# Kernel tuning notes

Measured on AMD Instinct MI355X. Metric: run time of the kernel, lower is better.

Reference implementation:

```python
import jax, jax.numpy as jnp
import numpy as np

T_NUM = 1024      # tracks
DET_NUM = 1024    # detections
DEG = 64          # candidate detections per track
E = T_NUM * DEG   # directed track->det edges (row<col half)
N = T_NUM + DET_NUM
D_IN = 512
D_EMB = 256
LAM = 5.0
SLACK = -0.2
SINKHORN_ITERS = 8


def setup_inputs() -> dict:
    key = jax.random.key(0)
    ks = jax.random.split(key, 20)
    x = jax.random.normal(ks[0], (N, D_IN), jnp.float32)
    coords = jax.random.uniform(ks[1], (N, 4), dtype=jnp.float32)
    r = jax.random.uniform(ks[2], (N, 4), dtype=jnp.float32)
    bx1 = r[:, 0] * 100.0; by1 = r[:, 1] * 100.0
    bw = r[:, 2] * 50.0 + 1.0; bh = r[:, 3] * 50.0 + 1.0
    coords_original = jnp.stack([bx1, by1, bx1 + bw, by1 + bh], axis=1)
    src_t = jnp.repeat(jnp.arange(T_NUM, dtype=jnp.int32), DEG)
    off = jnp.tile(jnp.arange(DEG, dtype=jnp.int32), T_NUM)
    dst_d = (src_t * 13 + off) % DET_NUM            # unique det per (track, slot)
    src = src_t
    dst = dst_d + T_NUM                              # detection node ids come after tracks
    edge_index = jnp.concatenate([jnp.stack([src, dst]), jnp.stack([dst, src])], axis=1)
    ground_truth = jax.random.bernoulli(ks[3], 0.1, (T_NUM * DET_NUM,)).astype(jnp.float32)

    def lin(k, i, o):
        return jax.random.normal(k, (i, o), jnp.float32) / np.sqrt(i).astype(np.float32)

    params = {
        'W_enc': lin(ks[4], D_IN, D_EMB), 'b_enc': jnp.zeros((D_EMB,), jnp.float32),
        'W1a': lin(ks[5], 2 * D_EMB, 64), 'b1a': jnp.zeros((64,), jnp.float32),
        'W2a': lin(ks[6], 64, 1), 'b2a': jnp.zeros((1,), jnp.float32),
        'W1g': lin(ks[7], 8, 16), 'b1g': jnp.zeros((16,), jnp.float32),
        'W2g': lin(ks[8], 16, 1), 'b2g': jnp.zeros((1,), jnp.float32),
        'W1f': lin(ks[9], 2, 8), 'b1f': jnp.zeros((8,), jnp.float32),
        'W2f': lin(ks[10], 8, 1), 'b2f': jnp.zeros((1,), jnp.float32),
        'Wn': lin(ks[11], D_EMB, D_EMB), 'Wm': lin(ks[12], D_EMB, D_EMB),
        'bo': jnp.zeros((D_EMB,), jnp.float32),
        'W1c': lin(ks[13], 2, 8), 'b1c': jnp.zeros((8,), jnp.float32),
        'W2c': lin(ks[14], 8, 1), 'b2c': jnp.zeros((1,), jnp.float32),
    }
    out = {'x': x, 'coords': coords, 'coords_original': coords_original,
           'ground_truth': ground_truth, 'edge_index': edge_index}
    out.update(params)
    return out


def _box_iou(a, b):
    # a, b: [E, 4] boxes (x1, y1, x2, y2)
    lt = jnp.maximum(a[:, :2], b[:, :2])
    rb = jnp.minimum(a[:, 2:], b[:, 2:])
    wh = jnp.clip(rb - lt, 0.0)
    inter = wh[:, 0] * wh[:, 1]
    area_a = (a[:, 2] - a[:, 0]) * (a[:, 3] - a[:, 1])
    area_b = (b[:, 2] - b[:, 0]) * (b[:, 3] - b[:, 1])
    return inter / (area_a + area_b - inter + 1e-9)


def _sinkhorn(M):
    def body(M, _):
        M = M / (jnp.sum(M, axis=1, keepdims=True) + 1e-9)
        M = M / (jnp.sum(M, axis=0, keepdims=True) + 1e-9)
        return M, None
    M, _ = jax.lax.scan(body, M, None, length=SINKHORN_ITERS)
    return M


def _forward(x, coords, coords_original,
             W_enc, b_enc, W1a, b1a, W2a, b2a, W1g, b1g, W2g, b2g,
             W1f, b1f, W2f, b2f, Wn, Wm, bo, W1c, b1c, W2c, b2c,
             edge_index):
    node = jax.nn.relu(x @ W_enc + b_enc)                      # [N, D_EMB]
    src, dst = edge_index[0], edge_index[1]                    # [2E]
    # batched per-edge appearance affinity (replaces python edge loop)
    pair = jnp.concatenate([node[src], node[dst]], axis=1)     # [2E, 2*D_EMB]
    a1 = jax.nn.relu(pair @ W1a + b1a) @ W2a + b2a             # [2E, 1]
    geo = jnp.concatenate([coords[src], coords[dst]], axis=1)  # [2E, 8]
    a2 = jax.nn.relu(geo @ W1g + b1g) @ W2g + b2g              # [2E, 1]
    e_in = jnp.concatenate([a1, a2], axis=1)                   # [2E, 2]
    edge_emb = jax.nn.relu(e_in @ W1f + b1f) @ W2f + b2f       # [2E, 1]
    # optim_net: one round of edge-weighted message passing
    msg = jax.ops.segment_sum(edge_emb * node[src], dst, num_segments=N)
    out = jax.nn.relu(node @ Wn + msg @ Wm + bo)               # [N, D_EMB]
    # forward (row < col) edges are the first E entries by construction
    sf, df = src[:E], dst[:E]
    oa, ob = out[sf], out[df]
    denom = jnp.maximum(jnp.linalg.norm(oa, axis=1) * jnp.linalg.norm(ob, axis=1), 1e-6)
    cosv = jnp.sum(oa * ob, axis=1) / denom                    # CosineSimilarity(dim=0) per edge
    iou = _box_iou(coords_original[sf], coords_original[df])   # [E]
    f_in = jnp.stack([cosv, iou], axis=1)                      # [E, 2]
    aff = (jax.nn.relu(f_in @ W1c + b1c) @ W2c + b2c)[:, 0]    # [E]
    # assignment matrix with slack row/col, scatter exp(aff*lam)
    slack_val = jnp.exp(jnp.float32(SLACK * LAM))
    M = jnp.full((T_NUM + 1, DET_NUM + 1), slack_val, jnp.float32)
    M = M.at[:T_NUM, :DET_NUM].set(0.0)
    M = M.at[sf, df - T_NUM].set(jnp.exp(aff * LAM))
    M = _sinkhorn(M)
    return M[:-1, :-1].reshape(-1)                             # [T_NUM*DET_NUM]


def reference(x, coords, coords_original, ground_truth, edge_index,
              W_enc, b_enc, W1a, b1a, W2a, b2a, W1g, b1g, W2g, b2g,
              W1f, b1f, W2f, b2f, Wn, Wm, bo, W1c, b1c, W2c, b2c):
    normalized_output = _forward(x, coords, coords_original,
                                 W_enc, b_enc, W1a, b1a, W2a, b2a,
                                 W1g, b1g, W2g, b2g, W1f, b1f, W2f, b2f,
                                 Wn, Wm, bo, W1c, b1c, W2c, b2c, edge_index)
    det_num = jnp.asarray(DET_NUM, jnp.int32)
    tracklet_num = jnp.asarray(T_NUM, jnp.int32)
    return (normalized_output, ground_truth, det_num, tracklet_num)
```

## Files before the change

kernel.cpp:

```cpp
#include <hip/hip_runtime.h>

#define T_NUM 1024
#define DET_NUM 1024
#define E_NUM 65536
#define TWO_E 131072
#define N_NODES 2048
#define D_IN 512
#define D_EMB 256

__device__ __forceinline__ unsigned bf16r(float x) {
  const unsigned u = __float_as_uint(x);
  return (u + 0x7fffu + ((u >> 16) & 1u)) >> 16;
}
__device__ __forceinline__ float bflo(unsigned p) { return __uint_as_float(p << 16); }
__device__ __forceinline__ float bfhi(unsigned p) { return __uint_as_float(p & 0xffff0000u); }

__global__ __launch_bounds__(1024) void k_enc_pg(
    const float* __restrict__ x, const float* __restrict__ W,
    const float* __restrict__ b, const float* __restrict__ coords,
    const float* __restrict__ W1a, const float* __restrict__ W1g,
    float* __restrict__ node, float* __restrict__ P1, float* __restrict__ P2,
    float* __restrict__ G1, float* __restrict__ G2) {
  __shared__ __align__(16) float ns[8][D_EMB];
  __shared__ __align__(16) float psq[3][8][D_EMB];
  __shared__ float pp1[8][64], pp2[8][64];
  const int tid = threadIdx.x;
  const int j = tid & 255;
  const int q = __builtin_amdgcn_readfirstlane(tid >> 8);
  const int row0 = blockIdx.x * 8;
  float acc[8];
  const float bj = b[j];
#pragma unroll
  for (int r = 0; r < 8; r++) acc[r] = (q == 0) ? bj : 0.f;
  const float* xr = x + (size_t)row0 * D_IN + q * 128;
  const float* Wp = W + (size_t)q * 128 * D_EMB;
  for (int k = 0; k < 128; k += 4) {
    const float w0 = Wp[(k + 0) * D_EMB + j];
    const float w1 = Wp[(k + 1) * D_EMB + j];
    const float w2 = Wp[(k + 2) * D_EMB + j];
    const float w3 = Wp[(k + 3) * D_EMB + j];
#pragma unroll
    for (int r = 0; r < 8; r++) {
      const float4 xv = *reinterpret_cast<const float4*>(xr + (size_t)r * D_IN + k);
      acc[r] = fmaf(xv.x, w0, acc[r]);
      acc[r] = fmaf(xv.y, w1, acc[r]);
      acc[r] = fmaf(xv.z, w2, acc[r]);
      acc[r] = fmaf(xv.w, w3, acc[r]);
    }
  }
  if (q > 0) {
#pragma unroll
    for (int r = 0; r < 8; r++) psq[q - 1][r][j] = acc[r];
  }
  __syncthreads();
  if (q == 0) {
#pragma unroll
    for (int r = 0; r < 8; r++) {
      const float v = fmaxf(acc[r] + psq[0][r][j] + psq[1][r][j] + psq[2][r][j], 0.f);
      node[(size_t)(row0 + r) * D_EMB + j] = v;
      ns[r][j] = v;
    }
  }
  __syncthreads();
  const int r2 = tid >> 7, q2 = (tid >> 6) & 1, hh = tid & 63;
  float a1 = 0.f, a2 = 0.f;
  {
    const int k0 = q2 * 128;
    for (int k = 0; k < 128; k += 4) {
      const float4 nv = *reinterpret_cast<const float4*>(&ns[r2][k0 + k]);
      a1 = fmaf(nv.x, W1a[(k0 + k + 0) * 64 + hh], a1);
      a1 = fmaf(nv.y, W1a[(k0 + k + 1) * 64 + hh], a1);
      a1 = fmaf(nv.z, W1a[(k0 + k + 2) * 64 + hh], a1);
      a1 = fmaf(nv.w, W1a[(k0 + k + 3) * 64 + hh], a1);
      a2 = fmaf(nv.x, W1a[(D_EMB + k0 + k + 0) * 64 + hh], a2);
      a2 = fmaf(nv.y, W1a[(D_EMB + k0 + k + 1) * 64 + hh], a2);
      a2 = fmaf(nv.z, W1a[(D_EMB + k0 + k + 2) * 64 + hh], a2);
      a2 = fmaf(nv.w, W1a[(D_EMB + k0 + k + 3) * 64 + hh], a2);
    }
    if (q2 == 1) { pp1[r2][hh] = a1; pp2[r2][hh] = a2; }
  }
  __syncthreads();
  if (q2 == 0) {
    P1[(size_t)(row0 + r2) * 64 + hh] = a1 + pp1[r2][hh];
    P2[(size_t)(row0 + r2) * 64 + hh] = a2 + pp2[r2][hh];
  }
  if (tid < 128) {
    const int r = tid >> 4, g = tid & 15;
    const int n = row0 + r;
    float g1 = 0.f, g2 = 0.f;
#pragma unroll
    for (int k = 0; k < 4; k++) {
      const float c = coords[(size_t)n * 4 + k];
      g1 = fmaf(c, W1g[k * 16 + g], g1);
      g2 = fmaf(c, W1g[(4 + k) * 16 + g], g2);
    }
    G1[(size_t)n * 16 + g] = g1;
    G2[(size_t)n * 16 + g] = g2;
  }
}

__global__ __launch_bounds__(512) void k_msg_out(
    const float* __restrict__ node,
    const float* __restrict__ P1, const float* __restrict__ P2,
    const float* __restrict__ G1, const float* __restrict__ G2,
    const float* __restrict__ b1a, const float* __restrict__ W2a, const float* __restrict__ b2a,
    const float* __restrict__ b1g, const float* __restrict__ W2g, const float* __restrict__ b2g,
    const float* __restrict__ W1f, const float* __restrict__ b1f,
    const float* __restrict__ W2f, const float* __restrict__ b2f,
    const float* __restrict__ Wn, const float* __restrict__ Wm,
    const float* __restrict__ bo, float* __restrict__ outE, float* __restrict__ nrm) {
  __shared__ __align__(16) float msp[4][2][D_EMB];
  __shared__ __align__(16) float ms[2][D_EMB];
  __shared__ float wsh[2][64];
  __shared__ int ssh[2][64];
  __shared__ float pa1[2][64], pa2[2][64];
  __shared__ __align__(16) float ph[2][D_EMB];
  __shared__ float redn[4][2];
  const int tid = threadIdx.x;
  const int h = __builtin_amdgcn_readfirstlane(tid >> 8);
  const int j = tid & 255;
  const int row0 = blockIdx.x * 2;
  float a1p = 0.f, a2p = 0.f;
  if (j < 128) {
    const int r = j >> 6, o = j & 63;
    const int n = row0 + r;
    int src;
    if (n < T_NUM) {
      src = T_NUM + ((13 * n + o) & 1023);
    } else {
      const int d = n - T_NUM;
      src = (709 * (d - o)) & 1023;
    }
    const float4* p1 = (const float4*)(P1 + (size_t)src * 64) + h * 8;
    const float4* p2 = (const float4*)(P2 + (size_t)n * 64) + h * 8;
    const float4* b1 = (const float4*)b1a + h * 8;
    const float4* w2 = (const float4*)W2a + h * 8;
#pragma unroll
    for (int i = 0; i < 8; i++) {
      const float4 pa = p1[i], pb = p2[i], bb = b1[i], ww = w2[i];
      a1p += fmaxf(pa.x + pb.x + bb.x, 0.f) * ww.x + fmaxf(pa.y + pb.y + bb.y, 0.f) * ww.y +
             fmaxf(pa.z + pb.z + bb.z, 0.f) * ww.z + fmaxf(pa.w + pb.w + bb.w, 0.f) * ww.w;
    }
    const float4* g1 = (const float4*)(G1 + (size_t)src * 16) + h * 2;
    const float4* g2 = (const float4*)(G2 + (size_t)n * 16) + h * 2;
    const float4* bg = (const float4*)b1g + h * 2;
    const float4* wg = (const float4*)W2g + h * 2;
#pragma unroll
    for (int i = 0; i < 2; i++) {
      const float4 pa = g1[i], pb = g2[i], bb = bg[i], ww = wg[i];
      a2p += fmaxf(pa.x + pb.x + bb.x, 0.f) * ww.x + fmaxf(pa.y + pb.y + bb.y, 0.f) * ww.y +
             fmaxf(pa.z + pb.z + bb.z, 0.f) * ww.z + fmaxf(pa.w + pb.w + bb.w, 0.f) * ww.w;
    }
    if (h == 1) { pa1[r][o] = a1p; pa2[r][o] = a2p; ssh[r][o] = src; }
  }
  __syncthreads();
  if (h == 0 && j < 128) {
    const int r = j >> 6, o = j & 63;
    const float a1 = a1p + pa1[r][o] + b2a[0];
    const float a2 = a2p + pa2[r][o] + b2g[0];
    float acc = b2f[0];
#pragma unroll
    for (int jj = 0; jj < 8; jj++) {
      const float hv = fmaxf(a1 * W1f[jj] + a2 * W1f[8 + jj] + b1f[jj], 0.f);
      acc = fmaf(hv, W2f[jj], acc);
    }
    wsh[r][o] = acc;
  }
  __syncthreads();
  {
    const int s = tid >> 7;
    const int r = (tid >> 6) & 1;
    const int qd = tid & 63;
    const int i0 = s * 16;
    float ax = 0.f, ay = 0.f, az = 0.f, aw = 0.f;
#pragma unroll 4
    for (int i = 0; i < 16; i++) {
      const float w = wsh[r][i0 + i];
      const float4 nv = *reinterpret_cast<const float4*>(
          node + (size_t)ssh[r][i0 + i] * D_EMB + 4 * qd);
      ax = fmaf(w, nv.x, ax); ay = fmaf(w, nv.y, ay);
      az = fmaf(w, nv.z, az); aw = fmaf(w, nv.w, aw);
    }
    *reinterpret_cast<float4*>(&msp[s][r][4 * qd]) = make_float4(ax, ay, az, aw);
  }
  __syncthreads();
  {
    const int r = tid >> 8, jj = tid & 255;
    ms[r][jj] = ((msp[0][r][jj] + msp[1][r][jj]) + msp[2][r][jj]) + msp[3][r][jj];
  }
  __syncthreads();
  float acc2[2];
  const float bj = bo[j];
#pragma unroll
  for (int rr = 0; rr < 2; rr++) acc2[rr] = (h == 0) ? bj : 0.f;
  const float* nrow = node + (size_t)row0 * D_EMB + h * 128;
  const float* Wnp = Wn + (size_t)h * 128 * D_EMB;
  const float* Wmp = Wm + (size_t)h * 128 * D_EMB;
  for (int k = 0; k < 128; k += 4) {
    const float wn0 = Wnp[(k + 0) * D_EMB + j], wm0 = Wmp[(k + 0) * D_EMB + j];
    const float wn1 = Wnp[(k + 1) * D_EMB + j], wm1 = Wmp[(k + 1) * D_EMB + j];
    const float wn2 = Wnp[(k + 2) * D_EMB + j], wm2 = Wmp[(k + 2) * D_EMB + j];
    const float wn3 = Wnp[(k + 3) * D_EMB + j], wm3 = Wmp[(k + 3) * D_EMB + j];
#pragma unroll
    for (int rr = 0; rr < 2; rr++) {
      const float4 nv = *reinterpret_cast<const float4*>(nrow + (size_t)rr * D_EMB + k);
      const float4 mv = *reinterpret_cast<const float4*>(&ms[rr][h * 128 + k]);
      acc2[rr] = fmaf(nv.x, wn0, acc2[rr]); acc2[rr] = fmaf(mv.x, wm0, acc2[rr]);
      acc2[rr] = fmaf(nv.y, wn1, acc2[rr]); acc2[rr] = fmaf(mv.y, wm1, acc2[rr]);
      acc2[rr] = fmaf(nv.z, wn2, acc2[rr]); acc2[rr] = fmaf(mv.z, wm2, acc2[rr]);
      acc2[rr] = fmaf(nv.w, wn3, acc2[rr]); acc2[rr] = fmaf(mv.w, wm3, acc2[rr]);
    }
  }
  if (h == 1) {
#pragma unroll
    for (int rr = 0; rr < 2; rr++) ph[rr][j] = acc2[rr];
  }
  __syncthreads();
  if (h == 0) {
    const int lane = tid & 63, wid = tid >> 6;
#pragma unroll
    for (int rr = 0; rr < 2; rr++) {
      acc2[rr] = fmaxf(acc2[rr] + ph[rr][j], 0.f);
      outE[(size_t)(row0 + rr) * D_EMB + j] = acc2[rr];
    }
#pragma unroll
    for (int rr = 0; rr < 2; rr++) {
      float sq = acc2[rr] * acc2[rr];
#pragma unroll
      for (int oo = 32; oo > 0; oo >>= 1) sq += __shfl_down(sq, oo, 64);
      if (lane == 0) redn[wid][rr] = sq;
    }
  }
  __syncthreads();
  if (tid < 2)
    nrm[row0 + tid] = sqrtf(redn[0][tid] + redn[1][tid] + redn[2][tid] + redn[3][tid]);
}

__global__ __launch_bounds__(256) void k_aff(
    const float* __restrict__ outE, const float* __restrict__ nrm,
    const float* __restrict__ cov,
    const float* __restrict__ W1c, const float* __restrict__ b1c,
    const float* __restrict__ W2c, const float* __restrict__ b2c,
    float* __restrict__ Kbp, unsigned short* __restrict__ KTg) {
  __shared__ __align__(16) float4 oas[64];
  __shared__ float psum[4][64];
  const int t = blockIdx.x;
  const int tid = threadIdx.x;
  const int o = tid & 63, c = tid >> 6;
  const int s = t;
  if (tid < 64) oas[tid] = ((const float4*)(outE + (size_t)s * D_EMB))[tid];
  __syncthreads();
  const int d = (13 * t + o) & 1023;
  const int dn = T_NUM + d;
  {
    const float4* ob = (const float4*)(outE + (size_t)dn * D_EMB) + c * 16;
    const float4* oa = oas + c * 16;
    float dot = 0.f;
#pragma unroll
    for (int i = 0; i < 16; i++) {
      const float4 a = oa[i], bq = ob[i];
      dot += a.x * bq.x + a.y * bq.y + a.z * bq.z + a.w * bq.w;
    }
    psum[c][o] = dot;
  }
  __syncthreads();
  if (tid < 64) {
    const float dot = psum[0][o] + psum[1][o] + psum[2][o] + psum[3][o];
    const float cosv = dot / fmaxf(nrm[s] * nrm[dn], 1e-6f);
    const float4 A = ((const float4*)cov)[s];
    const float4 B = ((const float4*)cov)[dn];
    const float ltx = fmaxf(A.x, B.x), lty = fmaxf(A.y, B.y);
    const float rbx = fminf(A.z, B.z), rby = fminf(A.w, B.w);
    const float wx = fmaxf(rbx - ltx, 0.f), wy = fmaxf(rby - lty, 0.f);
    const float inter = wx * wy;
    const float areaA = (A.z - A.x) * (A.w - A.y);
    const float areaB = (B.z - B.x) * (B.w - B.y);
    const float iou = inter / (areaA + areaB - inter + 1e-9f);
    float aff = b2c[0];
#pragma unroll
    for (int jj = 0; jj < 8; jj++) {
      const float h = fmaxf(cosv * W1c[jj] + iou * W1c[8 + jj] + b1c[jj], 0.f);
      aff = fmaf(h, W2c[jj], aff);
    }
    const float Kv = __expf(aff * 5.0f);
    const int tp = (13 * s) & 1023;
    Kbp[tp * 68 + (tp & 3) + o] = Kv;
    if (o < 4) {
      const int pr = (o < (tp & 3)) ? o : o + 64;
      Kbp[tp * 68 + pr] = 0.f;
    }
    const int cbase = (((d & 1022) + 960) & 1023) & ~3;
    const int rho = (((d + 961) & 1023) - cbase) & 1023;
    KTg[d * 72 + rho + 63 - o] = (unsigned short)bf16r(Kv);
    if (o < 8) {
      const int slot = (o < rho) ? o : o + 64;
      KTg[d * 72 + slot] = 0;
    }
  }
}

__global__ __launch_bounds__(512, 2) void k_sinkhorn(
    const float* __restrict__ Kbp, const unsigned short* __restrict__ KTg,
    float* __restrict__ ug, float* __restrict__ vg,
    const float* __restrict__ gt, float* __restrict__ out) {
  if (blockIdx.x != 0) {
    const size_t idx = (size_t)(blockIdx.x - 1) * 512 + threadIdx.x;
    ((float4*)out)[(size_t)T_NUM * 256 + idx] = ((const float4*)gt)[idx];
    return;
  }
  __shared__ __align__(16) float u_lds[1092];
  __shared__ __align__(16) float v_lds[1092];
  __shared__ float red_u[8];
  __shared__ float red_v[8];
  __shared__ __align__(16) uint4 ktlA[9][512];
  __shared__ __align__(16) uint4 ktlB[9][512];
  const int tid = threadIdx.x;
  const int lane = tid & 63, wid = tid >> 6;
  const int ra = 2 * tid, rb = 2 * tid + 1;
  const int qa = (ra & ~3) >> 2;
  const int cbase = ((ra + 960) & 1023) & ~3;
  const int qc = cbase >> 2;
  unsigned k0[34], k1[34];
  {
    const float4* s0p = (const float4*)(Kbp + (size_t)ra * 68);
    const float4* s1p = (const float4*)(Kbp + (size_t)rb * 68);
#pragma unroll
    for (int c = 0; c < 17; c++) {
      float4 f = s0p[c];
      k0[2 * c]     = bf16r(f.x) | (bf16r(f.y) << 16);
      k0[2 * c + 1] = bf16r(f.z) | (bf16r(f.w) << 16);
      f = s1p[c];
      k1[2 * c]     = bf16r(f.x) | (bf16r(f.y) << 16);
      k1[2 * c + 1] = bf16r(f.z) | (bf16r(f.w) << 16);
    }
  }
  {
    const uint4* g = (const uint4*)KTg;
#pragma unroll
    for (int q = 0; q < 9; q++) ktlA[q][tid] = g[tid * 18 + q];
#pragma unroll
    for (int q = 0; q < 9; q++) ktlB[q][tid] = g[tid * 18 + 9 + q];
  }
  float u0 = 1.f, u1 = 1.f, vc0 = 1.f, vc1 = 1.f, u_sl = 1.f, v_sl = 1.f;
  v_lds[tid] = 1.f; v_lds[tid + 512] = 1.f;
  if (tid < 68) v_lds[1024 + tid] = 1.f;
  if (tid < 8) red_v[tid] = 128.f;
  const float slack = 0.36787944117144233f;
  __syncthreads();
#pragma unroll 1
  for (int it = 0; it < 8; ++it) {
    const float4* vq = (const float4*)v_lds;
    float a00 = 0.f, a01 = 0.f, a10 = 0.f, a11 = 0.f;
#pragma unroll
    for (int c = 0; c < 17; c++) {
      const float4 v4 = vq[qa + c];
      unsigned p = k0[2 * c];
      a00 = fmaf(bflo(p), v4.x, a00); a00 = fmaf(bfhi(p), v4.y, a00);
      p = k0[2 * c + 1];
      a01 = fmaf(bflo(p), v4.z, a01); a01 = fmaf(bfhi(p), v4.w, a01);
      p = k1[2 * c];
      a10 = fmaf(bflo(p), v4.x, a10); a10 = fmaf(bfhi(p), v4.y, a10);
      p = k1[2 * c + 1];
      a11 = fmaf(bflo(p), v4.z, a11); a11 = fmaf(bfhi(p), v4.w, a11);
    }
    const float sumv = red_v[0] + red_v[1] + red_v[2] + red_v[3] +
                       red_v[4] + red_v[5] + red_v[6] + red_v[7];
    const float s0 = a00 + a01 + slack * v_sl;
    const float s1 = a10 + a11 + slack * v_sl;
    u0 = u0 / (u0 * s0 + 1e-9f);
    u1 = u1 / (u1 * s1 + 1e-9f);
    u_sl = u_sl / (u_sl * slack * (sumv + v_sl) + 1e-9f);
    u_lds[ra] = u0; u_lds[rb] = u1;
    if (tid < 34) { u_lds[1024 + ra] = u0; u_lds[1024 + rb] = u1; }
    float usum = u0 + u1;
#pragma unroll
    for (int o = 32; o > 0; o >>= 1) usum += __shfl_down(usum, o, 64);
    if (lane == 0) red_u[wid] = usum;
    __syncthreads();
    const float4* uq = (const float4*)u_lds;
    float t0 = 0.f, t1 = 0.f;
#pragma unroll 3
    for (int q = 0; q < 9; q++) {
      const uint4 A = ktlA[q][tid];
      const uint4 B = ktlB[q][tid];
      const float4 ua = uq[qc + 2 * q];
      const float4 ub = uq[qc + 2 * q + 1];
      t0 = fmaf(bflo(A.x), ua.x, t0); t0 = fmaf(bfhi(A.x), ua.y, t0);
      t0 = fmaf(bflo(A.y), ua.z, t0); t0 = fmaf(bfhi(A.y), ua.w, t0);
      t0 = fmaf(bflo(A.z), ub.x, t0); t0 = fmaf(bfhi(A.z), ub.y, t0);
      t0 = fmaf(bflo(A.w), ub.z, t0); t0 = fmaf(bfhi(A.w), ub.w, t0);
      t1 = fmaf(bflo(B.x), ua.x, t1); t1 = fmaf(bfhi(B.x), ua.y, t1);
      t1 = fmaf(bflo(B.y), ua.z, t1); t1 = fmaf(bfhi(B.y), ua.w, t1);
      t1 = fmaf(bflo(B.z), ub.x, t1); t1 = fmaf(bfhi(B.z), ub.y, t1);
      t1 = fmaf(bflo(B.w), ub.z, t1); t1 = fmaf(bfhi(B.w), ub.w, t1);
    }
    const float sumu = red_u[0] + red_u[1] + red_u[2] + red_u[3] +
                       red_u[4] + red_u[5] + red_u[6] + red_u[7];
    t0 += slack * u_sl;
    t1 += slack * u_sl;
    vc0 = vc0 / (vc0 * t0 + 1e-9f);
    vc1 = vc1 / (vc1 * t1 + 1e-9f);
    v_sl = v_sl / (v_sl * slack * (sumu + u_sl) + 1e-9f);
    v_lds[ra] = vc0; v_lds[rb] = vc1;
    if (tid < 34) { v_lds[1024 + ra] = vc0; v_lds[1024 + rb] = vc1; }
    float vsum = vc0 + vc1;
#pragma unroll
    for (int o = 32; o > 0; o >>= 1) vsum += __shfl_down(vsum, o, 64);
    if (lane == 0) red_v[wid] = vsum;
    __syncthreads();
  }
  ((float2*)ug)[tid] = make_float2(u0, u1);
  ((float2*)vg)[tid] = make_float2(vc0, vc1);
}

__global__ __launch_bounds__(256) void k_final(
    const float* __restrict__ Kbp, const float* __restrict__ ug,
    const float* __restrict__ vg, float* __restrict__ out) {
  const int t = blockIdx.x;
  const int tp = (13 * t) & 1023;
  const float u = ug[tp];
  const float* krow = Kbp + (size_t)tp * 68 + (tp & 3);
  const int d0 = threadIdx.x * 4;
  const float4 v4 = ((const float4*)vg)[threadIdx.x];
  float4 o4;
  const int m0 = (d0 - tp) & 1023;
  const int m1 = (d0 + 1 - tp) & 1023;
  const int m2 = (d0 + 2 - tp) & 1023;
  const int m3 = (d0 + 3 - tp) & 1023;
  o4.x = (m0 < 64) ? u * krow[m0] * v4.x : 0.f;
  o4.y = (m1 < 64) ? u * krow[m1] * v4.y : 0.f;
  o4.z = (m2 < 64) ? u * krow[m2] * v4.z : 0.f;
  o4.w = (m3 < 64) ? u * krow[m3] * v4.w : 0.f;
  ((float4*)out)[(size_t)t * 256 + threadIdx.x] = o4;
  if (t == 0 && threadIdx.x == 0) {
    out[(size_t)2 * T_NUM * DET_NUM] = 1024.0f;
    out[(size_t)2 * T_NUM * DET_NUM + 1] = 1024.0f;
  }
}

extern "C" void kernel_launch(void* const* d_in, const int* in_sizes, int n_in,
                              void* d_out, int out_size, void* d_ws, size_t ws_size,
                              hipStream_t stream) {
  const float* x      = (const float*)d_in[0];
  const float* coords = (const float*)d_in[1];
  const float* cov    = (const float*)d_in[2];
  const float* gt     = (const float*)d_in[3];
  const float* W_enc  = (const float*)d_in[5];
  const float* b_enc  = (const float*)d_in[6];
  const float* W1a    = (const float*)d_in[7];
  const float* b1a    = (const float*)d_in[8];
  const float* W2a    = (const float*)d_in[9];
  const float* b2a    = (const float*)d_in[10];
  const float* W1g    = (const float*)d_in[11];
  const float* b1g    = (const float*)d_in[12];
  const float* W2g    = (const float*)d_in[13];
  const float* b2g    = (const float*)d_in[14];
  const float* W1f    = (const float*)d_in[15];
  const float* b1f    = (const float*)d_in[16];
  const float* W2f    = (const float*)d_in[17];
  const float* b2f    = (const float*)d_in[18];
  const float* Wn     = (const float*)d_in[19];
  const float* Wm     = (const float*)d_in[20];
  const float* bo     = (const float*)d_in[21];
  const float* W1c    = (const float*)d_in[22];
  const float* b1c    = (const float*)d_in[23];
  const float* W2c    = (const float*)d_in[24];
  const float* b2c    = (const float*)d_in[25];

  char* ws = (char*)d_ws;
  size_t off = 0;
  auto alloc = [&](size_t bytes) {
    char* p = ws + off;
    off = (off + bytes + 255) & ~(size_t)255;
    return p;
  };
  float* node  = (float*)alloc((size_t)N_NODES * D_EMB * 4);
  float* P1    = (float*)alloc((size_t)N_NODES * 64 * 4);
  float* P2    = (float*)alloc((size_t)N_NODES * 64 * 4);
  float* G1    = (float*)alloc((size_t)N_NODES * 16 * 4);
  float* G2    = (float*)alloc((size_t)N_NODES * 16 * 4);
  float* outE  = (float*)alloc((size_t)N_NODES * D_EMB * 4);
  float* nrm   = (float*)alloc((size_t)N_NODES * 4);
  float* Kbp   = (float*)alloc((size_t)1024 * 68 * 4);
  unsigned short* KTg = (unsigned short*)alloc((size_t)1024 * 72 * 2);
  float* ug    = (float*)alloc(1024 * 4);
  float* vg    = (float*)alloc(1024 * 4);
  float* out   = (float*)d_out;

  k_enc_pg<<<N_NODES / 8, 1024, 0, stream>>>(x, W_enc, b_enc, coords, W1a, W1g,
                                             node, P1, P2, G1, G2);
  k_msg_out<<<N_NODES / 2, 512, 0, stream>>>(node, P1, P2, G1, G2,
                                             b1a, W2a, b2a, b1g, W2g, b2g,
                                             W1f, b1f, W2f, b2f,
                                             Wn, Wm, bo, outE, nrm);
  k_aff<<<T_NUM, 256, 0, stream>>>(outE, nrm, cov, W1c, b1c, W2c, b2c,
                                   Kbp, KTg);
  k_sinkhorn<<<513, 512, 0, stream>>>(Kbp, KTg, ug, vg, gt, out);
  k_final<<<T_NUM, 256, 0, stream>>>(Kbp, ug, vg, out);
}
```

Baseline: 210.7 us.

## Process four nodes per block in message/output kernel with K-split float4 GEMV

k_msg_out now handles four rows per block instead of two, halving the grid, so each Wn/Wm weight load is reused across four rows. The output GEMV is restructured: each wave takes a 32-wide K slice and computes float4 column outputs for all four rows, and the partial results are reduced through shared memory. Node rows are staged in LDS and all 512 threads now do the edge-weight computation. The cost is much more shared memory (about 44KB) and fewer blocks, which may lower occupancy and parallelism.

```diff
diff --git a/kernel.cpp b/kernel.cpp
--- a/kernel.cpp
+++ b/kernel.cpp
@@ -14,6 +14,10 @@
 }
 __device__ __forceinline__ float bflo(unsigned p) { return __uint_as_float(p << 16); }
 __device__ __forceinline__ float bfhi(unsigned p) { return __uint_as_float(p & 0xffff0000u); }
+__device__ __forceinline__ void fma4(float4& a, float s, const float4 w) {
+  a.x = fmaf(s, w.x, a.x); a.y = fmaf(s, w.y, a.y);
+  a.z = fmaf(s, w.z, a.z); a.w = fmaf(s, w.w, a.w);
+}
 
 __global__ __launch_bounds__(1024) void k_enc_pg(
     const float* __restrict__ x, const float* __restrict__ W,
@@ -109,20 +113,20 @@
     const float* __restrict__ W2f, const float* __restrict__ b2f,
     const float* __restrict__ Wn, const float* __restrict__ Wm,
     const float* __restrict__ bo, float* __restrict__ outE, float* __restrict__ nrm) {
-  __shared__ __align__(16) float msp[4][2][D_EMB];
-  __shared__ __align__(16) float ms[2][D_EMB];
-  __shared__ float wsh[2][64];
-  __shared__ int ssh[2][64];
-  __shared__ float pa1[2][64], pa2[2][64];
-  __shared__ __align__(16) float ph[2][D_EMB];
-  __shared__ float redn[4][2];
+  __shared__ __align__(16) float msp[2][4][D_EMB];
+  __shared__ __align__(16) float ms[4][D_EMB];
+  __shared__ __align__(16) float nsh[4][D_EMB];
+  __shared__ __align__(16) float pg[8][4][D_EMB];
+  __shared__ float wsh[4][64];
+  __shared__ int ssh[4][64];
+  __shared__ float pa1[4][64], pa2[4][64];
+  __shared__ float redn[8];
   const int tid = threadIdx.x;
   const int h = __builtin_amdgcn_readfirstlane(tid >> 8);
   const int j = tid & 255;
-  const int row0 = blockIdx.x * 2;
-  float a1p = 0.f, a2p = 0.f;
-  if (j < 128) {
-    const int r = j >> 6, o = j & 63;
+  const int row0 = blockIdx.x * 4;
+  {
+    const int r = (tid >> 6) & 3, o = tid & 63;
     const int n = row0 + r;
     int src;
     if (n < T_NUM) {
@@ -131,6 +135,7 @@
       const int d = n - T_NUM;
       src = (709 * (d - o)) & 1023;
     }
+    float a1p = 0.f, a2p = 0.f;
     const float4* p1 = (const float4*)(P1 + (size_t)src * 64) + h * 8;
     const float4* p2 = (const float4*)(P2 + (size_t)n * 64) + h * 8;
     const float4* b1 = (const float4*)b1a + h * 8;
@@ -152,12 +157,13 @@
              fmaxf(pa.z + pb.z + bb.z, 0.f) * ww.z + fmaxf(pa.w + pb.w + bb.w, 0.f) * ww.w;
     }
     if (h == 1) { pa1[r][o] = a1p; pa2[r][o] = a2p; ssh[r][o] = src; }
-  }
-  __syncthreads();
-  if (h == 0 && j < 128) {
-    const int r = j >> 6, o = j & 63;
-    const float a1 = a1p + pa1[r][o] + b2a[0];
-    const float a2 = a2p + pa2[r][o] + b2g[0];
+    else        { wsh[r][o] = a1p; pg[0][r][o] = a2p; }
+  }
+  __syncthreads();
+  if (h == 0) {
+    const int r = (tid >> 6) & 3, o = tid & 63;
+    const float a1 = wsh[r][o] + pa1[r][o] + b2a[0];
+    const float a2 = pg[0][r][o] + pa2[r][o] + b2g[0];
     float acc = b2f[0];
 #pragma unroll
     for (int jj = 0; jj < 8; jj++) {
@@ -165,16 +171,20 @@
       acc = fmaf(hv, W2f[jj], acc);
     }
     wsh[r][o] = acc;
-  }
-  __syncthreads();
-  {
-    const int s = tid >> 7;
-    const int r = (tid >> 6) & 1;
+  } else {
+#pragma unroll
+    for (int rr = 0; rr < 4; rr++)
+      nsh[rr][j] = node[(size_t)(row0 + rr) * D_EMB + j];
+  }
+  __syncthreads();
+  {
+    const int s = tid >> 8;
+    const int r = (tid >> 6) & 3;
     const int qd = tid & 63;
-    const int i0 = s * 16;
+    const int i0 = s * 32;
     float ax = 0.f, ay = 0.f, az = 0.f, aw = 0.f;
 #pragma unroll 4
-    for (int i = 0; i < 16; i++) {
+    for (int i = 0; i < 32; i++) {
       const float w = wsh[r][i0 + i];
       const float4 nv = *reinterpret_cast<const float4*>(
           node + (size_t)ssh[r][i0 + i] * D_EMB + 4 * qd);
@@ -185,55 +195,59 @@
   }
   __syncthreads();
   {
-    const int r = tid >> 8, jj = tid & 255;
-    ms[r][jj] = ((msp[0][r][jj] + msp[1][r][jj]) + msp[2][r][jj]) + msp[3][r][jj];
-  }
-  __syncthreads();
-  float acc2[2];
-  const float bj = bo[j];
-#pragma unroll
-  for (int rr = 0; rr < 2; rr++) acc2[rr] = (h == 0) ? bj : 0.f;
-  const float* nrow = node + (size_t)row0 * D_EMB + h * 128;
-  const float* Wnp = Wn + (size_t)h * 128 * D_EMB;
-  const float* Wmp = Wm + (size_t)h * 128 * D_EMB;
-  for (int k = 0; k < 128; k += 4) {
-    const float wn0 = Wnp[(k + 0) * D_EMB + j], wm0 = Wmp[(k + 0) * D_EMB + j];
-    const float wn1 = Wnp[(k + 1) * D_EMB + j], wm1 = Wmp[(k + 1) * D_EMB + j];
-    const float wn2 = Wnp[(k + 2) * D_EMB + j], wm2 = Wmp[(k + 2) * D_EMB + j];
-    const float wn3 = Wnp[(k + 3) * D_EMB + j], wm3 = Wmp[(k + 3) * D_EMB + j];
-#pragma unroll
-    for (int rr = 0; rr < 2; rr++) {
-      const float4 nv = *reinterpret_cast<const float4*>(nrow + (size_t)rr * D_EMB + k);
-      const float4 mv = *reinterpret_cast<const float4*>(&ms[rr][h * 128 + k]);
-      acc2[rr] = fmaf(nv.x, wn0, acc2[rr]); acc2[rr] = fmaf(mv.x, wm0, acc2[rr]);
-      acc2[rr] = fmaf(nv.y, wn1, acc2[rr]); acc2[rr] = fmaf(mv.y, wm1, acc2[rr]);
-      acc2[rr] = fmaf(nv.z, wn2, acc2[rr]); acc2[rr] = fmaf(mv.z, wm2, acc2[rr]);
-      acc2[rr] = fmaf(nv.w, wn3, acc2[rr]); acc2[rr] = fmaf(mv.w, wm3, acc2[rr]);
-    }
-  }
-  if (h == 1) {
-#pragma unroll
-    for (int rr = 0; rr < 2; rr++) ph[rr][j] = acc2[rr];
-  }
-  __syncthreads();
-  if (h == 0) {
+    float* m0 = &ms[0][0];
+    const float* s0 = &msp[0][0][0];
+    const float* s1 = &msp[1][0][0];
+    m0[tid] = s0[tid] + s1[tid];
+    m0[tid + 512] = s0[tid + 512] + s1[tid + 512];
+  }
+  __syncthreads();
+  {
+    const int kq = __builtin_amdgcn_readfirstlane(tid >> 6);
+    const int jq = tid & 63;
+    const float4* Wn4 = (const float4*)Wn;
+    const float4* Wm4 = (const float4*)Wm;
+    float4 a0 = make_float4(0.f, 0.f, 0.f, 0.f);
+    float4 a1 = a0, a2 = a0, a3 = a0;
+    const int kbeg = kq * 32;
+    for (int k = kbeg; k < kbeg + 32; ++k) {
+      const float4 wn = Wn4[k * 64 + jq];
+      const float4 wm = Wm4[k * 64 + jq];
+      const float n0 = nsh[0][k], m0v = ms[0][k];
+      const float n1 = nsh[1][k], m1v = ms[1][k];
+      const float n2 = nsh[2][k], m2v = ms[2][k];
+      const float n3 = nsh[3][k], m3v = ms[3][k];
+      fma4(a0, n0, wn); fma4(a0, m0v, wm);
+      fma4(a1, n1, wn); fma4(a1, m1v, wm);
+      fma4(a2, n2, wn); fma4(a2, m2v, wm);
+      fma4(a3, n3, wn); fma4(a3, m3v, wm);
+    }
+    *reinterpret_cast<float4*>(&pg[kq][0][4 * jq]) = a0;
+    *reinterpret_cast<float4*>(&pg[kq][1][4 * jq]) = a1;
+    *reinterpret_cast<float4*>(&pg[kq][2][4 * jq]) = a2;
+    *reinterpret_cast<float4*>(&pg[kq][3][4 * jq]) = a3;
+  }
+  __syncthreads();
+  {
+    const int r = tid >> 7, jc = tid & 127;
     const int lane = tid & 63, wid = tid >> 6;
-#pragma unroll
-    for (int rr = 0; rr < 2; rr++) {
-      acc2[rr] = fmaxf(acc2[rr] + ph[rr][j], 0.f);
-      outE[(size_t)(row0 + rr) * D_EMB + j] = acc2[rr];
-    }
-#pragma unroll
-    for (int rr = 0; rr < 2; rr++) {
-      float sq = acc2[rr] * acc2[rr];
-#pragma unroll
-      for (int oo = 32; oo > 0; oo >>= 1) sq += __shfl_down(sq, oo, 64);
-      if (lane == 0) redn[wid][rr] = sq;
-    }
-  }
-  __syncthreads();
-  if (tid < 2)
-    nrm[row0 + tid] = sqrtf(redn[0][tid] + redn[1][tid] + redn[2][tid] + redn[3][tid]);
+    float v0 = bo[2 * jc + 0], v1 = bo[2 * jc + 1];
+#pragma unroll
+    for (int kq = 0; kq < 8; kq++) {
+      v0 += pg[kq][r][2 * jc + 0];
+      v1 += pg[kq][r][2 * jc + 1];
+    }
+    v0 = fmaxf(v0, 0.f); v1 = fmaxf(v1, 0.f);
+    *reinterpret_cast<float2*>(outE + (size_t)(row0 + r) * D_EMB + 2 * jc) =
+        make_float2(v0, v1);
+    float sq = v0 * v0 + v1 * v1;
+#pragma unroll
+    for (int oo = 32; oo > 0; oo >>= 1) sq += __shfl_down(sq, oo, 64);
+    if (lane == 0) redn[wid] = sq;
+  }
+  __syncthreads();
+  if (tid < 4)
+    nrm[row0 + tid] = sqrtf(redn[2 * tid] + redn[2 * tid + 1]);
 }
 
 __global__ __launch_bounds__(256) void k_aff(
@@ -489,7 +503,7 @@
 
   k_enc_pg<<<N_NODES / 8, 1024, 0, stream>>>(x, W_enc, b_enc, coords, W1a, W1g,
                                              node, P1, P2, G1, G2);
-  k_msg_out<<<N_NODES / 2, 512, 0, stream>>>(node, P1, P2, G1, G2,
+  k_msg_out<<<N_NODES / 4, 512, 0, stream>>>(node, P1, P2, G1, G2,
                                              b1a, W2a, b2a, b1g, W2g, b2g,
                                              W1f, b1f, W2f, b2f,
                                              Wn, Wm, bo, outE, nrm);
```

Result: faster. 202.2 us (-4.0%).
